# Kernel tuning notes

Hardware: AMD Instinct MI355X
Metric: run time of the kernel (lower is better)

## Reference

```python
import jax, jax.numpy as jnp
import numpy as np

N, D, O, H, T, S, R, BN = 4096, 256, 256, 256, 512, 8, 4, 2  # nodes, in, out, hidden, text_len, adj_size, relations used, basis_num


def setup_inputs() -> dict:
    key = jax.random.key(0)
    ks = jax.random.split(key, 16)
    sc = 0.05
    return {
        "entity_embeddings": jax.random.normal(ks[0], (N, D), jnp.float32) * sc,
        "text_encodings": jax.random.normal(ks[1], (1, T, 2 * H), jnp.float32) * sc,
        "adj_to_use": jnp.arange(R, dtype=jnp.int32),
        "adj_masks": jax.random.randint(ks[2], (R, N, N), 0, 2, dtype=jnp.int32),
        "text_guids": jax.random.normal(ks[3], (S, 2 * H), jnp.float32) * sc,
        "graph_guids_1": jax.random.normal(ks[4], (S, D), jnp.float32) * sc,
        "graph_guids_2": jax.random.normal(ks[5], (S, D), jnp.float32) * sc,
        "guid_a": jax.random.normal(ks[6], (S,), jnp.float32),
        "basis_V": jax.random.normal(ks[7], (D, BN, O), jnp.float32) * sc,
        "basis_b": jax.random.normal(ks[8], (S, BN), jnp.float32) * sc,
        "W_1": jax.random.normal(ks[9], (2 * H, D), jnp.float32) * sc,
        "W_2": jax.random.normal(ks[10], (2 * H, D), jnp.float32) * sc,
        "ln_gamma": jnp.ones((O,), jnp.float32),
        "ln_beta": jnp.zeros((O,), jnp.float32),
    }


def reference(entity_embeddings, text_encodings, adj_to_use, adj_masks,
              text_guids, graph_guids_1, graph_guids_2, guid_a,
              basis_V, basis_b, W_1, W_2, ln_gamma, ln_beta):
    te = text_encodings[0]                                  # [T, 2H] (batch of 1)
    tg = text_guids[adj_to_use]                             # [R, 2H]
    # text attention: softmax over T, per relation
    att = jax.nn.softmax(te @ tg.T, axis=0)                 # [T, R]
    context = att.T @ te                                    # [R, 2H]
    c1 = context @ W_1                                      # [R, D]
    c2 = context @ W_2
    ga = jax.nn.sigmoid(guid_a[adj_to_use])[:, None]        # [R, 1]
    g1 = ga * graph_guids_1[adj_to_use] + (1.0 - ga) * c1   # [R, D]
    g2 = ga * graph_guids_2[adj_to_use] + (1.0 - ga) * c2
    s1 = entity_embeddings @ g1.T                           # [N, R]
    s2 = entity_embeddings @ g2.T
    # A[r,i,j] = s1[i,r] + s2[j,r], masked softmax over j
    A = s1.T[:, :, None] + s2.T[:, None, :]                 # [R, N, N]
    A = jnp.where(adj_masks == 1, A, jnp.float32(-1e10))
    A = jax.nn.softmax(A, axis=-1)
    fused = jnp.einsum('rij,jd->rid', A, entity_embeddings) # [R, N, D]
    # torch.cat over relations on last dim -> column index r*D + d
    fused_cat = jnp.transpose(fused, (1, 0, 2)).reshape(N, R * D)
    # torch.matmul([R,BN],[D,BN,O]) -> [D,R,O], then .view(R*D, O) (row index d*R + r)
    bb = basis_b[adj_to_use]                                # [R, BN]
    W = jnp.einsum('rb,dbo->dro', bb, basis_V).reshape(D * R, O)
    out = fused_cat @ W                                     # [N, O]
    mu = jnp.mean(out, axis=-1, keepdims=True)
    var = jnp.var(out, axis=-1, keepdims=True)
    out = (out - mu) / jnp.sqrt(var + 1e-5) * ln_gamma + ln_beta
    return jax.nn.relu(out)
```

## Files before the change

kernel.cpp:

```cpp
#include <hip/hip_runtime.h>
#include <hip/hip_bf16.h>


typedef unsigned short u16;
typedef short bf16x8 __attribute__((ext_vector_type(8)));
typedef float f32x4 __attribute__((ext_vector_type(4)));
typedef int   v4i   __attribute__((ext_vector_type(4)));
typedef unsigned int v2u __attribute__((ext_vector_type(2)));

#define G2_OFF    0
#define E2_OFF    4096
#define WRT_OFF   69632
#define FPT_OFF   593920
#define FUSED_OFF 9506816
#define CAN_OFF   26284032

#define C_ENT 0
#define C_TE  1048576
#define C_TG  1310720
#define C_GG2 1314816
#define C_GA  1316864
#define C_BV  1316872
#define C_BB  1447944
#define C_W2  1447960
#define C_GAM 1579032
#define C_BET 1579288

__device__ __forceinline__ float b2f(u16 u) {
    union { unsigned int i; float f; } v; v.i = ((unsigned int)u) << 16; return v.f;
}
__device__ __forceinline__ u16 f2b(float f) {
    union { float f; unsigned int i; } v; v.f = f;
    return (u16)((v.i + 0x7FFFu + ((v.i >> 16) & 1u)) >> 16);
}

__global__ __launch_bounds__(256) void k_cvt(
    const void* s0, const void* s1, const void* s2, const void* s3,
    const void* s4, const void* s5, const void* s6, const void* s7,
    const void* s8, const void* s9, const unsigned* __restrict__ graw,
    u16* __restrict__ dst)
{
    bool isbf = (graw[0] == 0x3F803F80u);
    const void* srcs[10] = {s0, s1, s2, s3, s4, s5, s6, s7, s8, s9};
    const int ns[10]     = {1048576, 262144, 4096, 2048, 8, 131072, 16, 131072, 256, 256};
    const int offs[10]   = {C_ENT, C_TE, C_TG, C_GG2, C_GA, C_BV, C_BB, C_W2, C_GAM, C_BET};
    const int bstart[11] = {0, 512, 640, 642, 643, 644, 708, 709, 773, 774, 775};
    int b = blockIdx.x, a = 0;
    while (b >= bstart[a + 1]) ++a;
    int rel = b - bstart[a];
    int n = ns[a];
    u16* d = dst + offs[a];
    int base = rel * 2048 + threadIdx.x;
    if (isbf) {
        const u16* s = (const u16*)srcs[a];
        for (int k = 0; k < 8; ++k) { int i = base + k * 256; if (i < n) d[i] = s[i]; }
    } else {
        const float* s = (const float*)srcs[a];
        for (int k = 0; k < 8; ++k) { int i = base + k * 256; if (i < n) d[i] = f2b(s[i]); }
    }
}

__global__ __launch_bounds__(1024) void k_pre(const u16* __restrict__ te,
                                              const int* __restrict__ adj,
                                              const u16* __restrict__ tguids,
                                              const u16* __restrict__ gg2,
                                              const u16* __restrict__ guida,
                                              const u16* __restrict__ W2,
                                              float* __restrict__ g2ws) {
    __shared__ float s_tg[4 * 512];
    __shared__ float s_att[512 * 4];
    __shared__ float s_red[512 * 4];
    __shared__ float s_ctx[4 * 512];
    int tid = threadIdx.x;
    int a[4] = {adj[0], adj[1], adj[2], adj[3]};
    for (int idx = tid; idx < 2048; idx += 1024) {
        int r = idx >> 9, h = idx & 511;
        s_tg[r * 512 + h] = b2f(tguids[a[r] * 512 + h]);
    }
    __syncthreads();
    if (tid < 512) {
        float s[4] = {0.f, 0.f, 0.f, 0.f};
        const u16* row = te + tid * 512;
        for (int h = 0; h < 512; ++h) {
            float tv = b2f(row[h]);
            s[0] += tv * s_tg[h]; s[1] += tv * s_tg[512 + h];
            s[2] += tv * s_tg[1024 + h]; s[3] += tv * s_tg[1536 + h];
        }
        for (int r = 0; r < 4; ++r) { s_att[tid * 4 + r] = s[r]; s_red[tid * 4 + r] = s[r]; }
    }
    __syncthreads();
    for (int st = 256; st > 0; st >>= 1) {
        if (tid < st) for (int r = 0; r < 4; ++r)
            s_red[tid * 4 + r] = fmaxf(s_red[tid * 4 + r], s_red[(tid + st) * 4 + r]);
        __syncthreads();
    }
    float mx[4]; for (int r = 0; r < 4; ++r) mx[r] = s_red[r];
    __syncthreads();
    if (tid < 512) for (int r = 0; r < 4; ++r) {
        float e = __expf(s_att[tid * 4 + r] - mx[r]);
        s_att[tid * 4 + r] = e; s_red[tid * 4 + r] = e;
    }
    __syncthreads();
    for (int st = 256; st > 0; st >>= 1) {
        if (tid < st) for (int r = 0; r < 4; ++r)
            s_red[tid * 4 + r] += s_red[(tid + st) * 4 + r];
        __syncthreads();
    }
    float dn[4]; for (int r = 0; r < 4; ++r) dn[r] = s_red[r];
    __syncthreads();
    if (tid < 512) for (int r = 0; r < 4; ++r) s_att[tid * 4 + r] /= dn[r];
    __syncthreads();
    for (int rep = 0; rep < 2; ++rep) {
        int o = tid + rep * 1024; int r = o >> 9, h = o & 511;
        float acc = 0.f;
        for (int t = 0; t < 512; ++t) acc += s_att[t * 4 + r] * b2f(te[t * 512 + h]);
        s_ctx[r * 512 + h] = acc;
    }
    __syncthreads();
    {
        int r = tid >> 8, d = tid & 255;
        float acc = 0.f;
        for (int h = 0; h < 512; ++h) acc += s_ctx[r * 512 + h] * b2f(W2[h * 256 + d]);
        float gav = 1.f / (1.f + expf(-b2f(guida[a[r]])));
        g2ws[r * 256 + d] = gav * b2f(gg2[a[r] * 256 + d]) + (1.f - gav) * acc;
    }
}

__global__ __launch_bounds__(256) void k_s2_wrt(const u16* __restrict__ entity,
                                                const int* __restrict__ adj,
                                                const u16* __restrict__ basisV,
                                                const u16* __restrict__ basisb,
                                                const float* __restrict__ g2ws,
                                                float* __restrict__ e2ws,
                                                u16* __restrict__ wrt) {
    int b = blockIdx.x, tid = threadIdx.x;
    if (b < 64) {
        int j = b * 64 + (tid >> 2), r = tid & 3;
        const u16* erow = entity + j * 256;
        const float* g2r = g2ws + r * 256;
        float acc = 0.f;
        for (int d = 0; d < 256; ++d) acc += b2f(erow[d]) * g2r[d];
        e2ws[r * 4096 + j] = expf(acc);
    } else {
        int b2 = b - 64; int r = b2 >> 6;
        int c = (b2 & 63) * 4 + (tid >> 6);
        int dq = tid & 63;
        int dbase = dq * 4;
        int a[4] = {adj[0], adj[1], adj[2], adj[3]};
        for (int dd = 0; dd < 4; ++dd) {
            float w = 0.f;
            for (int bi = 0; bi < 2; ++bi)
                w += b2f(basisb[a[dd] * 2 + bi]) * b2f(basisV[((64 * r + dq) * 2 + bi) * 256 + c]);
            wrt[(r * 256 + c) * 256 + dbase + dd] = f2b(w);
        }
    }
}

__global__ __launch_bounds__(256) void k_fplus(const u16* __restrict__ entity,
                                               const u16* __restrict__ wrt,
                                               const float* __restrict__ e2ws,
                                               u16* __restrict__ fpt) {
    int b = blockIdx.x, tid = threadIdx.x;
    if (b < 256) {
        int r = b & 3, ct = (b >> 2) & 3, jt = b >> 4;
        int c0 = ct * 64, j0 = jt * 256;
        __shared__ __align__(16) u16 lw[64 * 264];
        const u16* wr = wrt + (r * 256 + c0) * 256;
        for (int k = 0; k < 8; ++k) {
            int ci = tid + k * 256; int row = ci >> 5, off = (ci & 31) * 8;
            *(v4i*)(&lw[row * 264 + off]) = *(const v4i*)(wr + row * 256 + off);
        }
        __syncthreads();
        int wave = tid >> 6, ln = tid & 15, q = (tid & 63) >> 4;
        f32x4 acc[4][4] = {};
        for (int ks = 0; ks < 8; ++ks) {
            bf16x8 afr[4], bfr[4];
            for (int mt = 0; mt < 4; ++mt)
                afr[mt] = *(const bf16x8*)(&lw[(mt * 16 + ln) * 264 + ks * 32 + q * 8]);
            for (int nt = 0; nt < 4; ++nt) {
                int j = j0 + (wave * 4 + nt) * 16 + ln;
                bfr[nt] = *(const bf16x8*)(entity + j * 256 + ks * 32 + q * 8);
            }
            for (int mt = 0; mt < 4; ++mt)
                for (int nt = 0; nt < 4; ++nt)
                    acc[mt][nt] = __builtin_amdgcn_mfma_f32_16x16x32_bf16(afr[mt], bfr[nt], acc[mt][nt], 0, 0, 0);
        }
        for (int nt = 0; nt < 4; ++nt) {
            int j = j0 + (wave * 4 + nt) * 16 + ln;
            float e2j = e2ws[r * 4096 + j];
            int kt = j >> 5, kk = j & 31;
            u16* dst = fpt + (((size_t)(r * 128 + kt)) * 272 << 5);
            for (int mt = 0; mt < 4; ++mt)
                for (int reg = 0; reg < 4; ++reg) {
                    int c = c0 + mt * 16 + q * 4 + reg;
                    dst[(c << 5) + kk] = f2b(acc[mt][nt][reg] * e2j);
                }
        }
    } else {
        int b2 = b - 256; int r = b2 >> 1, half = b2 & 1;
        const float* e2r = e2ws + r * 4096;
        for (int it = 0; it < 128; ++it) {
            int l = it * 256 + tid;
            int kk = l & 31;
            int c  = 256 + ((l >> 5) & 15);
            int kt = half * 64 + (l >> 9);
            fpt[(((size_t)(r * 128 + kt) * 272 + c) << 5) + kk] =
                (c == 256) ? f2b(e2r[kt * 32 + kk]) : (u16)0;
        }
    }
}

__global__ __launch_bounds__(512) void k_big(const int* __restrict__ masks,
                                             const u16* __restrict__ fpt,
                                             float* __restrict__ fused) {
    __shared__ __align__(16) u16 lm[64 * 40];
    __shared__ __align__(16) u16 lf[272 * 40];
    __shared__ float lden[64];
    int b = blockIdx.x, tid = threadIdx.x;
    int xcd = b & 7; int r = xcd & 3;
    int it = (b >> 3) + ((xcd >> 2) << 5);
    long i0 = (long)it * 64;
    const int* mbase = masks + ((long)r << 24) + i0 * 4096;
    const u16* fbase = fpt + (size_t)r * 128 * 272 * 32;
    int mrow = tid >> 3, mch = tid & 7;
    int wave = tid >> 6, lane = tid & 63, ln = lane & 15, q = lane >> 4;
    int mg = wave >> 2, ng = wave & 3;

    f32x4 acc[2][4] = {};
    f32x4 accD0 = {}, accD1 = {};

    v4i pmA, pf0A, pf1A, pf2A, pmB, pf0B, pf1B, pf2B;
    auto load_into = [&](int kt, v4i& pm_, v4i& p0, v4i& p1, v4i& p2) {
        pm_ = __builtin_nontemporal_load((const v4i*)(mbase + mrow * 4096 + kt * 32 + mch * 4));
        const u16* su = fbase + (size_t)kt * 8704;
        p0 = *(const v4i*)(su + tid * 8);
        p1 = *(const v4i*)(su + (tid + 512) * 8);
        if (tid < 64) p2 = *(const v4i*)(su + (tid + 1024) * 8);
    };
    auto step = [&](int kt, v4i& pm_, v4i& p0, v4i& p1, v4i& p2) {
        __syncthreads();
        {
            unsigned int m0 = (unsigned)pm_.x * 0x3F80u, m1 = (unsigned)pm_.y * 0x3F80u;
            unsigned int m2 = (unsigned)pm_.z * 0x3F80u, m3 = (unsigned)pm_.w * 0x3F80u;
            v2u w; w.x = m0 | (m1 << 16); w.y = m2 | (m3 << 16);
            *(v2u*)(&lm[mrow * 40 + mch * 4]) = w;
        }
        *(v4i*)(&lf[(tid >> 2) * 40 + (tid & 3) * 8]) = p0;
        { int ci = tid + 512; *(v4i*)(&lf[(ci >> 2) * 40 + (ci & 3) * 8]) = p1; }
        if (tid < 64) { int ci = tid + 1024; *(v4i*)(&lf[(ci >> 2) * 40 + (ci & 3) * 8]) = p2; }
        __syncthreads();
        if (kt + 2 < 128) load_into(kt + 2, pm_, p0, p1, p2);
        bf16x8 a0 = *(const bf16x8*)(&lm[(mg * 32 + ln) * 40 + q * 8]);
        bf16x8 a1 = *(const bf16x8*)(&lm[(mg * 32 + 16 + ln) * 40 + q * 8]);
        #pragma unroll
        for (int nt = 0; nt < 4; ++nt) {
            bf16x8 bf = *(const bf16x8*)(&lf[((ng * 4 + nt) * 16 + ln) * 40 + q * 8]);
            acc[0][nt] = __builtin_amdgcn_mfma_f32_16x16x32_bf16(a0, bf, acc[0][nt], 0, 0, 0);
            acc[1][nt] = __builtin_amdgcn_mfma_f32_16x16x32_bf16(a1, bf, acc[1][nt], 0, 0, 0);
        }
        if (ng == 3) {
            bf16x8 bf = *(const bf16x8*)(&lf[(256 + ln) * 40 + q * 8]);
            accD0 = __builtin_amdgcn_mfma_f32_16x16x32_bf16(a0, bf, accD0, 0, 0, 0);
            accD1 = __builtin_amdgcn_mfma_f32_16x16x32_bf16(a1, bf, accD1, 0, 0, 0);
        }
    };

    load_into(0, pmA, pf0A, pf1A, pf2A);
    load_into(1, pmB, pf0B, pf1B, pf2B);
    #pragma unroll 1
    for (int kt = 0; kt < 128; kt += 2) {
        step(kt,     pmA, pf0A, pf1A, pf2A);
        step(kt + 1, pmB, pf0B, pf1B, pf2B);
    }

    if (ng == 3 && ln == 0) {
        #pragma unroll
        for (int reg = 0; reg < 4; ++reg) {
            lden[mg * 32 + q * 4 + reg]      = accD0[reg];
            lden[mg * 32 + 16 + q * 4 + reg] = accD1[reg];
        }
    }
    __syncthreads();
    float* fb = fused + ((long)r * 4096 + i0) * 256;
    #pragma unroll
    for (int mt = 0; mt < 2; ++mt) {
        float rd[4];
        #pragma unroll
        for (int reg = 0; reg < 4; ++reg) rd[reg] = 1.0f / lden[mg * 32 + mt * 16 + q * 4 + reg];
        #pragma unroll
        for (int nt = 0; nt < 4; ++nt) {
            int c = (ng * 4 + nt) * 16 + ln;
            #pragma unroll
            for (int reg = 0; reg < 4; ++reg) {
                int row = mg * 32 + mt * 16 + q * 4 + reg;
                __builtin_nontemporal_store(acc[mt][nt][reg] * rd[reg], fb + row * 256 + c);
            }
        }
    }
}

__global__ __launch_bounds__(256) void k_ln(const float* __restrict__ fused,
                                            const u16* __restrict__ gamma,
                                            const u16* __restrict__ beta,
                                            const unsigned* __restrict__ graw,
                                            void* __restrict__ outraw) {
    __shared__ float red[256];
    int i = blockIdx.x, o = threadIdx.x;
    float x = 0.f;
    for (int r = 0; r < 4; ++r)
        x += __builtin_nontemporal_load(fused + ((long)(r << 12) + i) * 256 + o);
    red[o] = x; __syncthreads();
    for (int st = 128; st > 0; st >>= 1) { if (o < st) red[o] += red[o + st]; __syncthreads(); }
    float mu = red[0] * (1.f / 256.f);
    __syncthreads();
    float v = x - mu;
    red[o] = v * v; __syncthreads();
    for (int st = 128; st > 0; st >>= 1) { if (o < st) red[o] += red[o + st]; __syncthreads(); }
    float var = red[0] * (1.f / 256.f);
    float y = v * rsqrtf(var + 1e-5f) * b2f(gamma[o]) + b2f(beta[o]);
    float res = fmaxf(y, 0.f);
    bool isbf = (graw[0] == 0x3F803F80u);
    if (isbf) ((u16*)outraw)[i * 256 + o] = f2b(res);
    else      ((float*)outraw)[i * 256 + o] = res;
}

extern "C" void kernel_launch(void* const* d_in, const int* in_sizes, int n_in,
                              void* d_out, int out_size, void* d_ws, size_t ws_size,
                              hipStream_t stream) {
    const int* adj   = (const int*)d_in[2];
    const int* masks = (const int*)d_in[3];
    const unsigned* graw = (const unsigned*)d_in[12];
    char* ws = (char*)d_ws;
    float* g2ws = (float*)(ws + G2_OFF);
    float* e2ws = (float*)(ws + E2_OFF);
    u16*   wrt  = (u16*)(ws + WRT_OFF);
    u16*   fpt  = (u16*)(ws + FPT_OFF);
    float* fus  = (float*)(ws + FUSED_OFF);
    u16*   can  = (u16*)(ws + CAN_OFF);

    k_cvt<<<775, 256, 0, stream>>>(d_in[0], d_in[1], d_in[4], d_in[6], d_in[7],
                                   d_in[8], d_in[9], d_in[11], d_in[12], d_in[13],
                                   graw, can);
    const u16* entity = can + C_ENT;
    const u16* te     = can + C_TE;
    const u16* tguids = can + C_TG;
    const u16* gg2    = can + C_GG2;
    const u16* guida  = can + C_GA;
    const u16* basisV = can + C_BV;
    const u16* basisb = can + C_BB;
    const u16* W2     = can + C_W2;
    const u16* gamma  = can + C_GAM;
    const u16* beta   = can + C_BET;

    k_pre<<<1, 1024, 0, stream>>>(te, adj, tguids, gg2, guida, W2, g2ws);
    k_s2_wrt<<<320, 256, 0, stream>>>(entity, adj, basisV, basisb, g2ws, e2ws, wrt);
    k_fplus<<<264, 256, 0, stream>>>(entity, wrt, e2ws, fpt);
    k_big<<<256, 512, 0, stream>>>(masks, fpt, fus);
    k_ln<<<4096, 256, 0, stream>>>(fus, gamma, beta, graw, d_out);
}
```

Measured before the change: 551.0 us.

## Deepen mask prefetch pipeline and vectorize small pre/post kernels

The main masked-softmax GEMM kernel now keeps four k-tiles of mask and feature loads in flight instead of two, to hide more global-memory latency on the large mask stream. The single-block text-attention kernel splits its dot products across all threads and uses vectorized bf16 loads with shuffle reductions. The s2 kernel computes all four relations per thread from shared memory, and the layernorm kernel replaces its shared-memory tree reductions with wave shuffles. The deeper prefetch raises register pressure in the main kernel, which may lower occupancy.

```diff
diff --git a/kernel.cpp b/kernel.cpp
--- a/kernel.cpp
+++ b/kernel.cpp
@@ -71,6 +71,7 @@
     __shared__ float s_att[512 * 4];
     __shared__ float s_red[512 * 4];
     __shared__ float s_ctx[4 * 512];
+    __shared__ float s_part[1024 * 4];
     int tid = threadIdx.x;
     int a[4] = {adj[0], adj[1], adj[2], adj[3]};
     for (int idx = tid; idx < 2048; idx += 1024) {
@@ -78,15 +79,30 @@
         s_tg[r * 512 + h] = b2f(tguids[a[r] * 512 + h]);
     }
     __syncthreads();
+    {
+        int t = tid & 511, half = tid >> 9;
+        int h0 = half * 256;
+        float s0 = 0.f, s1 = 0.f, s2 = 0.f, s3 = 0.f;
+        const u16* row = te + t * 512 + h0;
+        for (int hb = 0; hb < 256; hb += 8) {
+            bf16x8 v = *(const bf16x8*)(row + hb);
+            #pragma unroll
+            for (int k = 0; k < 8; ++k) {
+                float tv = b2f((u16)v[k]);
+                int h = h0 + hb + k;
+                s0 += tv * s_tg[h];        s1 += tv * s_tg[512 + h];
+                s2 += tv * s_tg[1024 + h]; s3 += tv * s_tg[1536 + h];
+            }
+        }
+        s_part[tid * 4 + 0] = s0; s_part[tid * 4 + 1] = s1;
+        s_part[tid * 4 + 2] = s2; s_part[tid * 4 + 3] = s3;
+    }
+    __syncthreads();
     if (tid < 512) {
-        float s[4] = {0.f, 0.f, 0.f, 0.f};
-        const u16* row = te + tid * 512;
-        for (int h = 0; h < 512; ++h) {
-            float tv = b2f(row[h]);
-            s[0] += tv * s_tg[h]; s[1] += tv * s_tg[512 + h];
-            s[2] += tv * s_tg[1024 + h]; s[3] += tv * s_tg[1536 + h];
-        }
-        for (int r = 0; r < 4; ++r) { s_att[tid * 4 + r] = s[r]; s_red[tid * 4 + r] = s[r]; }
+        for (int r = 0; r < 4; ++r) {
+            float s = s_part[tid * 4 + r] + s_part[(512 + tid) * 4 + r];
+            s_att[tid * 4 + r] = s; s_red[tid * 4 + r] = s;
+        }
     }
     __syncthreads();
     for (int st = 256; st > 0; st >>= 1) {
@@ -110,11 +126,26 @@
     __syncthreads();
     if (tid < 512) for (int r = 0; r < 4; ++r) s_att[tid * 4 + r] /= dn[r];
     __syncthreads();
-    for (int rep = 0; rep < 2; ++rep) {
-        int o = tid + rep * 1024; int r = o >> 9, h = o & 511;
-        float acc = 0.f;
-        for (int t = 0; t < 512; ++t) acc += s_att[t * 4 + r] * b2f(te[t * 512 + h]);
-        s_ctx[r * 512 + h] = acc;
+    {
+        int u = tid >> 2, tq = tid & 3;
+        int r = u >> 6, h0 = (u & 63) * 8;
+        float acc[8] = {};
+        int t0 = tq * 128;
+        for (int t = t0; t < t0 + 128; ++t) {
+            bf16x8 v = *(const bf16x8*)(te + t * 512 + h0);
+            float at = s_att[t * 4 + r];
+            #pragma unroll
+            for (int k = 0; k < 8; ++k) acc[k] += at * b2f((u16)v[k]);
+        }
+        #pragma unroll
+        for (int k = 0; k < 8; ++k) {
+            acc[k] += __shfl_xor(acc[k], 1);
+            acc[k] += __shfl_xor(acc[k], 2);
+        }
+        if (tq == 0) {
+            #pragma unroll
+            for (int k = 0; k < 8; ++k) s_ctx[r * 512 + h0 + k] = acc[k];
+        }
     }
     __syncthreads();
     {
@@ -134,15 +165,26 @@
                                                 float* __restrict__ e2ws,
                                                 u16* __restrict__ wrt) {
     int b = blockIdx.x, tid = threadIdx.x;
-    if (b < 64) {
-        int j = b * 64 + (tid >> 2), r = tid & 3;
+    if (b < 16) {
+        __shared__ float sg2[1024];
+        for (int i = tid; i < 1024; i += 256) sg2[i] = g2ws[i];
+        __syncthreads();
+        int j = b * 256 + tid;
         const u16* erow = entity + j * 256;
-        const float* g2r = g2ws + r * 256;
-        float acc = 0.f;
-        for (int d = 0; d < 256; ++d) acc += b2f(erow[d]) * g2r[d];
-        e2ws[r * 4096 + j] = expf(acc);
+        float a0 = 0.f, a1 = 0.f, a2 = 0.f, a3 = 0.f;
+        for (int d0 = 0; d0 < 256; d0 += 8) {
+            bf16x8 v = *(const bf16x8*)(erow + d0);
+            #pragma unroll
+            for (int k = 0; k < 8; ++k) {
+                float ev = b2f((u16)v[k]);
+                a0 += ev * sg2[d0 + k];       a1 += ev * sg2[256 + d0 + k];
+                a2 += ev * sg2[512 + d0 + k]; a3 += ev * sg2[768 + d0 + k];
+            }
+        }
+        e2ws[j] = expf(a0); e2ws[4096 + j] = expf(a1);
+        e2ws[8192 + j] = expf(a2); e2ws[12288 + j] = expf(a3);
     } else {
-        int b2 = b - 64; int r = b2 >> 6;
+        int b2 = b - 16; int r = b2 >> 6;
         int c = (b2 & 63) * 4 + (tid >> 6);
         int dq = tid & 63;
         int dbase = dq * 4;
@@ -229,27 +271,28 @@
     f32x4 acc[2][4] = {};
     f32x4 accD0 = {}, accD1 = {};
 
-    v4i pmA, pf0A, pf1A, pf2A, pmB, pf0B, pf1B, pf2B;
-    auto load_into = [&](int kt, v4i& pm_, v4i& p0, v4i& p1, v4i& p2) {
-        pm_ = __builtin_nontemporal_load((const v4i*)(mbase + mrow * 4096 + kt * 32 + mch * 4));
+    struct Slot { v4i pm, p0, p1, p2; };
+    Slot sA, sB, sC, sD;
+    auto load_into = [&](int kt, Slot& s) {
+        s.pm = __builtin_nontemporal_load((const v4i*)(mbase + mrow * 4096 + kt * 32 + mch * 4));
         const u16* su = fbase + (size_t)kt * 8704;
-        p0 = *(const v4i*)(su + tid * 8);
-        p1 = *(const v4i*)(su + (tid + 512) * 8);
-        if (tid < 64) p2 = *(const v4i*)(su + (tid + 1024) * 8);
+        s.p0 = *(const v4i*)(su + tid * 8);
+        s.p1 = *(const v4i*)(su + (tid + 512) * 8);
+        if (tid < 64) s.p2 = *(const v4i*)(su + (tid + 1024) * 8);
     };
-    auto step = [&](int kt, v4i& pm_, v4i& p0, v4i& p1, v4i& p2) {
+    auto step = [&](int kt, Slot& s) {
         __syncthreads();
         {
-            unsigned int m0 = (unsigned)pm_.x * 0x3F80u, m1 = (unsigned)pm_.y * 0x3F80u;
-            unsigned int m2 = (unsigned)pm_.z * 0x3F80u, m3 = (unsigned)pm_.w * 0x3F80u;
+            unsigned int m0 = (unsigned)s.pm.x * 0x3F80u, m1 = (unsigned)s.pm.y * 0x3F80u;
+            unsigned int m2 = (unsigned)s.pm.z * 0x3F80u, m3 = (unsigned)s.pm.w * 0x3F80u;
             v2u w; w.x = m0 | (m1 << 16); w.y = m2 | (m3 << 16);
             *(v2u*)(&lm[mrow * 40 + mch * 4]) = w;
         }
-        *(v4i*)(&lf[(tid >> 2) * 40 + (tid & 3) * 8]) = p0;
-        { int ci = tid + 512; *(v4i*)(&lf[(ci >> 2) * 40 + (ci & 3) * 8]) = p1; }
-        if (tid < 64) { int ci = tid + 1024; *(v4i*)(&lf[(ci >> 2) * 40 + (ci & 3) * 8]) = p2; }
-        __syncthreads();
-        if (kt + 2 < 128) load_into(kt + 2, pm_, p0, p1, p2);
+        *(v4i*)(&lf[(tid >> 2) * 40 + (tid & 3) * 8]) = s.p0;
+        { int ci = tid + 512; *(v4i*)(&lf[(ci >> 2) * 40 + (ci & 3) * 8]) = s.p1; }
+        if (tid < 64) { int ci = tid + 1024; *(v4i*)(&lf[(ci >> 2) * 40 + (ci & 3) * 8]) = s.p2; }
+        __syncthreads();
+        if (kt + 4 < 128) load_into(kt + 4, s);
         bf16x8 a0 = *(const bf16x8*)(&lm[(mg * 32 + ln) * 40 + q * 8]);
         bf16x8 a1 = *(const bf16x8*)(&lm[(mg * 32 + 16 + ln) * 40 + q * 8]);
         #pragma unroll
@@ -265,12 +308,16 @@
         }
     };
 
-    load_into(0, pmA, pf0A, pf1A, pf2A);
-    load_into(1, pmB, pf0B, pf1B, pf2B);
+    load_into(0, sA);
+    load_into(1, sB);
+    load_into(2, sC);
+    load_into(3, sD);
     #pragma unroll 1
-    for (int kt = 0; kt < 128; kt += 2) {
-        step(kt,     pmA, pf0A, pf1A, pf2A);
-        step(kt + 1, pmB, pf0B, pf1B, pf2B);
+    for (int kt = 0; kt < 128; kt += 4) {
+        step(kt,     sA);
+        step(kt + 1, sB);
+        step(kt + 2, sC);
+        step(kt + 3, sD);
     }
 
     if (ng == 3 && ln == 0) {
@@ -304,19 +351,25 @@
                                             const u16* __restrict__ beta,
                                             const unsigned* __restrict__ graw,
                                             void* __restrict__ outraw) {
-    __shared__ float red[256];
+    __shared__ float part[8];
     int i = blockIdx.x, o = threadIdx.x;
     float x = 0.f;
     for (int r = 0; r < 4; ++r)
         x += __builtin_nontemporal_load(fused + ((long)(r << 12) + i) * 256 + o);
-    red[o] = x; __syncthreads();
-    for (int st = 128; st > 0; st >>= 1) { if (o < st) red[o] += red[o + st]; __syncthreads(); }
-    float mu = red[0] * (1.f / 256.f);
-    __syncthreads();
+    float s = x;
+    #pragma unroll
+    for (int st = 32; st > 0; st >>= 1) s += __shfl_xor(s, st);
+    int w = o >> 6;
+    if ((o & 63) == 0) part[w] = s;
+    __syncthreads();
+    float mu = (part[0] + part[1] + part[2] + part[3]) * (1.f / 256.f);
     float v = x - mu;
-    red[o] = v * v; __syncthreads();
-    for (int st = 128; st > 0; st >>= 1) { if (o < st) red[o] += red[o + st]; __syncthreads(); }
-    float var = red[0] * (1.f / 256.f);
+    float qv = v * v;
+    #pragma unroll
+    for (int st = 32; st > 0; st >>= 1) qv += __shfl_xor(qv, st);
+    if ((o & 63) == 0) part[4 + w] = qv;
+    __syncthreads();
+    float var = (part[4] + part[5] + part[6] + part[7]) * (1.f / 256.f);
     float y = v * rsqrtf(var + 1e-5f) * b2f(gamma[o]) + b2f(beta[o]);
     float res = fmaxf(y, 0.f);
     bool isbf = (graw[0] == 0x3F803F80u);
@@ -353,7 +406,7 @@
     const u16* beta   = can + C_BET;
 
     k_pre<<<1, 1024, 0, stream>>>(te, adj, tguids, gg2, guida, W2, g2ws);
-    k_s2_wrt<<<320, 256, 0, stream>>>(entity, adj, basisV, basisb, g2ws, e2ws, wrt);
+    k_s2_wrt<<<272, 256, 0, stream>>>(entity, adj, basisV, basisb, g2ws, e2ws, wrt);
     k_fplus<<<264, 256, 0, stream>>>(entity, wrt, e2ws, fpt);
     k_big<<<256, 512, 0, stream>>>(masks, fpt, fus);
     k_ln<<<4096, 256, 0, stream>>>(fus, gamma, beta, graw, d_out);
```

Result: no change. 552.5 us (+0.3%).
